# Optimization experiments

Measured on AMD Instinct MI355X. Metric: run time of the kernel, lower is better.

## Reference

```python
import jax, jax.numpy as jnp
import numpy as np

N_NODES = 100000
N_EDGES = 1600000
D_IN = 128
D_HID = 128


def setup_inputs() -> dict:
    key = jax.random.key(0)
    ks = jax.random.split(key, 8)
    x = jax.random.normal(ks[0], (N_NODES, D_IN), dtype=jnp.float32)
    edge_index = jax.random.randint(ks[1], (2, N_EDGES), 0, N_NODES, dtype=jnp.int64)
    def glorot(k, fan_in, fan_out):
        s = jnp.sqrt(6.0 / (fan_in + fan_out))
        return jax.random.uniform(k, (fan_in, fan_out), jnp.float32, -s, s)
    return {
        "x": x,
        "edge_index": edge_index,
        "W1": glorot(ks[2], D_IN, D_HID), "b1": jnp.zeros((D_HID,), jnp.float32),
        "W2": glorot(ks[3], D_HID, D_HID), "b2": jnp.zeros((D_HID,), jnp.float32),
        "W3": glorot(ks[4], D_HID, D_HID), "b3": jnp.zeros((D_HID,), jnp.float32),
    }


def _gcn_conv(x, src, dst, norm, W, b, n_nodes):
    # x: [N, d_in] -> [N, d_out]; PyG GCNConv: scatter(norm * (xW)[src] -> dst) + b
    h = x @ W                                    # [N, d_out]
    msg = h[src] * norm[:, None]                 # [E+N, d_out] gathered messages
    out = jax.ops.segment_sum(msg, dst, num_segments=n_nodes)
    return out + b


def _norm_and_loops(edge_index, n_nodes):
    # add self-loops, compute symmetric normalization deg^-1/2[src]*deg^-1/2[dst]
    loop = jnp.arange(n_nodes, dtype=edge_index.dtype)
    src = jnp.concatenate([edge_index[0], loop])
    dst = jnp.concatenate([edge_index[1], loop])
    deg = jax.ops.segment_sum(jnp.ones_like(dst, dtype=jnp.float32), dst,
                              num_segments=n_nodes)
    dinv = jnp.where(deg > 0, jax.lax.rsqrt(deg), 0.0)
    norm = dinv[src] * dinv[dst]                 # [E+N]
    return src, dst, norm


def reference(x, edge_index, W1, b1, W2, b2, W3, b3):
    n = x.shape[0]
    src, dst, norm = _norm_and_loops(edge_index, n)
    h = jax.nn.relu(_gcn_conv(x, src, dst, norm, W1, b1, n))
    h = jax.nn.relu(_gcn_conv(h, src, dst, norm, W2, b2, n))
    return _gcn_conv(h, src, dst, norm, W3, b3, n)
```

## Files before the change

### kernel.cpp

```cpp
#include <hip/hip_runtime.h>

#define D 128

typedef __attribute__((ext_vector_type(8))) short bf16x8;
typedef __attribute__((ext_vector_type(4))) float f32x4;

union Frag {
    unsigned short s[8];
    uint4 u;
    bf16x8 v;
};

__device__ inline unsigned short bf16_rne(float x) {
    unsigned u = __float_as_uint(x);
    return (unsigned short)((u + 0x7fffu + ((u >> 16) & 1)) >> 16);
}

__global__ void detect64_k(const int* __restrict__ raw, int* __restrict__ flag) {
    __shared__ int bad;
    if (threadIdx.x == 0) bad = 0;
    __syncthreads();
    for (int i = threadIdx.x; i < 4096; i += 256)
        if (raw[2 * i + 1] != 0) bad = 1;
    __syncthreads();
    if (threadIdx.x == 0) *flag = bad ? 0 : 1;
}

__global__ void hist_k(const int* __restrict__ raw, const int* __restrict__ flag,
                       int* __restrict__ cnt, int E) {
    bool is64 = (*flag != 0);
    int S = gridDim.x * blockDim.x;
    int i = blockIdx.x * blockDim.x + threadIdx.x;
    for (; i + 3 * S < E; i += 4 * S) {
        int d0 = is64 ? raw[2 * (E + i)]         : raw[E + i];
        int d1 = is64 ? raw[2 * (E + i + S)]     : raw[E + i + S];
        int d2 = is64 ? raw[2 * (E + i + 2 * S)] : raw[E + i + 2 * S];
        int d3 = is64 ? raw[2 * (E + i + 3 * S)] : raw[E + i + 3 * S];
        atomicAdd(&cnt[d0], 1);
        atomicAdd(&cnt[d1], 1);
        atomicAdd(&cnt[d2], 1);
        atomicAdd(&cnt[d3], 1);
    }
    for (; i < E; i += S) {
        int d = is64 ? raw[2 * (E + i)] : raw[E + i];
        atomicAdd(&cnt[d], 1);
    }
}

__global__ void dinv_k(const int* __restrict__ cnt, float* __restrict__ dinv, int n) {
    int i = blockIdx.x * blockDim.x + threadIdx.x;
    if (i < n) dinv[i] = rsqrtf((float)cnt[i] + 1.0f);
}

__global__ void scan1_k(const int* __restrict__ cnt, int* __restrict__ rp,
                        int* __restrict__ part, int n) {
    __shared__ int s[256];
    int t = threadIdx.x;
    int base = blockIdx.x * 1024 + t * 4;
    int v0 = 0, v1 = 0, v2 = 0, v3 = 0;
    if (base + 0 < n) v0 = cnt[base + 0];
    if (base + 1 < n) v1 = cnt[base + 1];
    if (base + 2 < n) v2 = cnt[base + 2];
    if (base + 3 < n) v3 = cnt[base + 3];
    int sum = v0 + v1 + v2 + v3;
    s[t] = sum;
    __syncthreads();
    for (int off = 1; off < 256; off <<= 1) {
        int xv = 0;
        if (t >= off) xv = s[t - off];
        __syncthreads();
        s[t] += xv;
        __syncthreads();
    }
    int run = s[t] - sum;
    if (base + 0 < n) rp[base + 0] = run; run += v0;
    if (base + 1 < n) rp[base + 1] = run; run += v1;
    if (base + 2 < n) rp[base + 2] = run; run += v2;
    if (base + 3 < n) rp[base + 3] = run;
    if (t == 255) part[blockIdx.x] = s[255];
}

__global__ void scan2_k(int* __restrict__ part, int nb) {
    if (nb <= 256) {
        __shared__ int s[256];
        int t = threadIdx.x;
        int v = (t < nb) ? part[t] : 0;
        s[t] = v;
        __syncthreads();
        for (int off = 1; off < 256; off <<= 1) {
            int xv = 0;
            if (t >= off) xv = s[t - off];
            __syncthreads();
            s[t] += xv;
            __syncthreads();
        }
        if (t < nb) part[t] = s[t] - v;
    } else if (threadIdx.x == 0) {
        int run = 0;
        for (int i = 0; i < nb; i++) { int v = part[i]; part[i] = run; run += v; }
    }
}

__global__ void scan3_k(int* __restrict__ rp, int* __restrict__ cursor,
                        const int* __restrict__ part, int n, int E) {
    int i = blockIdx.x * blockDim.x + threadIdx.x;
    if (i < n) {
        int v = rp[i] + part[i >> 10];
        rp[i] = v;
        cursor[i] = v;
    }
    if (i == 0) rp[n] = E;
}

__global__ void build_k(const int* __restrict__ raw, const int* __restrict__ flag,
                        const float* __restrict__ dinv,
                        int* __restrict__ cursor, int2* __restrict__ csr, int E) {
    bool is64 = (*flag != 0);
    int S = gridDim.x * blockDim.x;
    int i = blockIdx.x * blockDim.x + threadIdx.x;
    for (; i + 3 * S < E; i += 4 * S) {
        int i0 = i, i1 = i + S, i2 = i + 2 * S, i3 = i + 3 * S;
        int s0 = is64 ? raw[2 * i0] : raw[i0];
        int s1 = is64 ? raw[2 * i1] : raw[i1];
        int s2 = is64 ? raw[2 * i2] : raw[i2];
        int s3 = is64 ? raw[2 * i3] : raw[i3];
        int d0 = is64 ? raw[2 * (E + i0)] : raw[E + i0];
        int d1 = is64 ? raw[2 * (E + i1)] : raw[E + i1];
        int d2 = is64 ? raw[2 * (E + i2)] : raw[E + i2];
        int d3 = is64 ? raw[2 * (E + i3)] : raw[E + i3];
        int p0 = atomicAdd(&cursor[d0], 1);
        int p1 = atomicAdd(&cursor[d1], 1);
        int p2 = atomicAdd(&cursor[d2], 1);
        int p3 = atomicAdd(&cursor[d3], 1);
        float w0 = dinv[s0] * dinv[d0];
        float w1 = dinv[s1] * dinv[d1];
        float w2 = dinv[s2] * dinv[d2];
        float w3 = dinv[s3] * dinv[d3];
        csr[p0] = make_int2(s0, __float_as_int(w0));
        csr[p1] = make_int2(s1, __float_as_int(w1));
        csr[p2] = make_int2(s2, __float_as_int(w2));
        csr[p3] = make_int2(s3, __float_as_int(w3));
    }
    for (; i < E; i += S) {
        int s = is64 ? raw[2 * i] : raw[i];
        int d = is64 ? raw[2 * (E + i)] : raw[E + i];
        int pos = atomicAdd(&cursor[d], 1);
        float w = dinv[s] * dinv[d];
        csr[pos] = make_int2(s, __float_as_int(w));
    }
}

__global__ void pack_k(const float* __restrict__ W, uint4* __restrict__ whi,
                       uint4* __restrict__ wlo) {
    int id = blockIdx.x * 256 + threadIdx.x;
    if (id >= 2048) return;
    int lane = id & 63, st = id >> 6;
    int s = st >> 3, t = st & 7;
    int col = t * 16 + (lane & 15);
    int kb = s * 32 + ((lane >> 4) & 3) * 8;
    Frag H, L;
#pragma unroll
    for (int j = 0; j < 8; ++j) {
        float x = W[(size_t)(kb + j) * D + col];
        unsigned u = __float_as_uint(x);
        unsigned r = (u + 0x7fffu + ((u >> 16) & 1)) & 0xffff0000u;
        H.s[j] = (unsigned short)(r >> 16);
        L.s[j] = bf16_rne(x - __uint_as_float(r));
    }
    whi[st * 64 + lane] = H.u;
    wlo[st * 64 + lane] = L.u;
}

template <int PRE>
__global__ __launch_bounds__(256) void gemm_mfma_k(const float* __restrict__ A,
        const uint4* __restrict__ whi, const uint4* __restrict__ wlo,
        float* __restrict__ H, int M) {
    int wv = threadIdx.x >> 6, lane = threadIdx.x & 63;
    int row0 = blockIdx.x * 64 + wv * 16;
    int arow = row0 + (lane & 15);
    if (arow >= M) arow = M - 1;
    const float* ap = A + (size_t)arow * D + ((lane >> 4) & 3) * 8;
    f32x4 acc[8];
#pragma unroll
    for (int t = 0; t < 8; ++t) acc[t] = (f32x4){0.f, 0.f, 0.f, 0.f};
#pragma unroll
    for (int s = 0; s < 4; ++s) {
        float4 a0 = *(const float4*)(ap + s * 32);
        float4 a1 = *(const float4*)(ap + s * 32 + 4);
        float av[8] = {a0.x, a0.y, a0.z, a0.w, a1.x, a1.y, a1.z, a1.w};
        Frag Ah, Al;
#pragma unroll
        for (int j = 0; j < 8; ++j) {
            float x = av[j];
            if (PRE) x = fmaxf(x, 0.f);
            unsigned u = __float_as_uint(x);
            unsigned r = (u + 0x7fffu + ((u >> 16) & 1)) & 0xffff0000u;
            Ah.s[j] = (unsigned short)(r >> 16);
            Al.s[j] = bf16_rne(x - __uint_as_float(r));
        }
        const uint4* wh = whi + (size_t)s * 8 * 64 + lane;
        const uint4* wl = wlo + (size_t)s * 8 * 64 + lane;
#pragma unroll
        for (int t = 0; t < 8; ++t) {
            Frag Bh, Bl;
            Bh.u = wh[t * 64];
            Bl.u = wl[t * 64];
            acc[t] = __builtin_amdgcn_mfma_f32_16x16x32_bf16(Ah.v, Bh.v, acc[t], 0, 0, 0);
            acc[t] = __builtin_amdgcn_mfma_f32_16x16x32_bf16(Al.v, Bh.v, acc[t], 0, 0, 0);
            acc[t] = __builtin_amdgcn_mfma_f32_16x16x32_bf16(Ah.v, Bl.v, acc[t], 0, 0, 0);
        }
    }
    int g = (lane >> 4) & 3, c = lane & 15;
#pragma unroll
    for (int r = 0; r < 4; ++r) {
        int row = row0 + g * 4 + r;
        if (row < M) {
#pragma unroll
            for (int t = 0; t < 8; ++t)
                H[(size_t)row * D + t * 16 + c] = acc[t][r];
        }
    }
}

__global__ __launch_bounds__(256) void agg_k(const float* __restrict__ h,
                                             const float* __restrict__ dinv,
                                             const int* __restrict__ rp,
                                             const int2* __restrict__ csr,
                                             const float* __restrict__ bias,
                                             float* __restrict__ out, int n) {
    int node = (blockIdx.x << 2) + (threadIdx.x >> 6);
    int lane = threadIdx.x & 63;
    if (node >= n) return;
    const float2* h2 = (const float2*)h;
    float2 b2 = ((const float2*)bias)[lane];
    float dn = dinv[node];
    float2 hv = h2[(size_t)node * 64 + lane];
    float sl = dn * dn;
    float accx = b2.x + sl * hv.x;
    float accy = b2.y + sl * hv.y;
    int e = rp[node], e1 = rp[node + 1];
    for (; e + 8 <= e1; e += 8) {
        int2 p0 = csr[e + 0], p1 = csr[e + 1], p2 = csr[e + 2], p3 = csr[e + 3];
        int2 p4 = csr[e + 4], p5 = csr[e + 5], p6 = csr[e + 6], p7 = csr[e + 7];
        float2 v0 = h2[(size_t)p0.x * 64 + lane];
        float2 v1 = h2[(size_t)p1.x * 64 + lane];
        float2 v2 = h2[(size_t)p2.x * 64 + lane];
        float2 v3 = h2[(size_t)p3.x * 64 + lane];
        float2 v4 = h2[(size_t)p4.x * 64 + lane];
        float2 v5 = h2[(size_t)p5.x * 64 + lane];
        float2 v6 = h2[(size_t)p6.x * 64 + lane];
        float2 v7 = h2[(size_t)p7.x * 64 + lane];
        float w0 = __int_as_float(p0.y), w1 = __int_as_float(p1.y);
        float w2 = __int_as_float(p2.y), w3 = __int_as_float(p3.y);
        float w4 = __int_as_float(p4.y), w5 = __int_as_float(p5.y);
        float w6 = __int_as_float(p6.y), w7 = __int_as_float(p7.y);
        accx += w0 * v0.x + w1 * v1.x + w2 * v2.x + w3 * v3.x
              + w4 * v4.x + w5 * v5.x + w6 * v6.x + w7 * v7.x;
        accy += w0 * v0.y + w1 * v1.y + w2 * v2.y + w3 * v3.y
              + w4 * v4.y + w5 * v5.y + w6 * v6.y + w7 * v7.y;
    }
    for (; e + 4 <= e1; e += 4) {
        int2 p0 = csr[e + 0], p1 = csr[e + 1], p2 = csr[e + 2], p3 = csr[e + 3];
        float2 v0 = h2[(size_t)p0.x * 64 + lane];
        float2 v1 = h2[(size_t)p1.x * 64 + lane];
        float2 v2 = h2[(size_t)p2.x * 64 + lane];
        float2 v3 = h2[(size_t)p3.x * 64 + lane];
        float w0 = __int_as_float(p0.y), w1 = __int_as_float(p1.y);
        float w2 = __int_as_float(p2.y), w3 = __int_as_float(p3.y);
        accx += w0 * v0.x + w1 * v1.x + w2 * v2.x + w3 * v3.x;
        accy += w0 * v0.y + w1 * v1.y + w2 * v2.y + w3 * v3.y;
    }
    for (; e < e1; ++e) {
        int2 p0 = csr[e];
        float w0 = __int_as_float(p0.y);
        float2 v0 = h2[(size_t)p0.x * 64 + lane];
        accx += w0 * v0.x;
        accy += w0 * v0.y;
    }
    float2 o; o.x = accx; o.y = accy;
    ((float2*)out)[(size_t)node * 64 + lane] = o;
}

extern "C" void kernel_launch(void* const* d_in, const int* in_sizes, int n_in,
                              void* d_out, int out_size, void* d_ws, size_t ws_size,
                              hipStream_t stream) {
    const float* x  = (const float*)d_in[0];
    const int* eraw = (const int*)d_in[1];
    const float* W1 = (const float*)d_in[2];
    const float* b1 = (const float*)d_in[3];
    const float* W2 = (const float*)d_in[4];
    const float* b2 = (const float*)d_in[5];
    const float* W3 = (const float*)d_in[6];
    const float* b3 = (const float*)d_in[7];
    int N = in_sizes[0] / D;
    int E = in_sizes[1] / 2;
    float* out = (float*)d_out;

    char* w = (char*)d_ws;
    float* h    = (float*)w; w += (size_t)N * D * 4;
    int2* csr   = (int2*)w;  w += (size_t)E * 8;
    int* cnt    = (int*)w;   w += (size_t)N * 4;
    float* dinv = (float*)w; w += (size_t)N * 4;
    int* rp     = (int*)w;   w += (size_t)(N + 1) * 4;
    int* cursor = (int*)w;   w += (size_t)N * 4;
    int* part   = (int*)w;   w += 1024 * 4;
    int* flag   = (int*)w;   w += 16;
    uint4* whi[3]; uint4* wlo[3];
    for (int l = 0; l < 3; ++l) {
        whi[l] = (uint4*)w; w += 2048 * 16;
        wlo[l] = (uint4*)w; w += 2048 * 16;
    }

    detect64_k<<<1, 256, 0, stream>>>(eraw, flag);
    hipMemsetAsync(cnt, 0, (size_t)N * 4, stream);
    hist_k<<<512, 256, 0, stream>>>(eraw, flag, cnt, E);
    dinv_k<<<(N + 255) / 256, 256, 0, stream>>>(cnt, dinv, N);
    int nb = (N + 1023) / 1024;
    scan1_k<<<nb, 256, 0, stream>>>(cnt, rp, part, N);
    scan2_k<<<1, 256, 0, stream>>>(part, nb);
    scan3_k<<<(N + 255) / 256, 256, 0, stream>>>(rp, cursor, part, N, E);
    build_k<<<512, 256, 0, stream>>>(eraw, flag, dinv, cursor, csr, E);

    pack_k<<<8, 256, 0, stream>>>(W1, whi[0], wlo[0]);
    pack_k<<<8, 256, 0, stream>>>(W2, whi[1], wlo[1]);
    pack_k<<<8, 256, 0, stream>>>(W3, whi[2], wlo[2]);

    int gb = (N + 63) / 64;
    int ab = (N + 3) / 4;
    gemm_mfma_k<0><<<gb, 256, 0, stream>>>(x, whi[0], wlo[0], h, N);
    agg_k<<<ab, 256, 0, stream>>>(h, dinv, rp, csr, b1, out, N);
    gemm_mfma_k<1><<<gb, 256, 0, stream>>>(out, whi[1], wlo[1], h, N);
    agg_k<<<ab, 256, 0, stream>>>(h, dinv, rp, csr, b2, out, N);
    gemm_mfma_k<1><<<gb, 256, 0, stream>>>(out, whi[2], wlo[2], h, N);
    agg_k<<<ab, 256, 0, stream>>>(h, dinv, rp, csr, b3, out, N);
}
```

Measured before the change: 739.5 us.

## Store intermediate features in bf16 and shrink CSR to source-only indices

The GEMM output h is now written as bf16, which halves the bytes the gather-heavy aggregation reads per neighbor. The CSR drops the precomputed edge weight and stores only the source index; aggregation recomputes the weight as dinv[src]*dinv[node], trading an extra small gather for less CSR traffic. The three weight-packing launches are merged into one, and the 4-edge unrolled tail loop is removed. Rounding h to bf16 loses precision and could push results close to the tolerance.

```diff
diff --git a/kernel.cpp b/kernel.cpp
--- a/kernel.cpp
+++ b/kernel.cpp
@@ -113,8 +113,7 @@
 }
 
 __global__ void build_k(const int* __restrict__ raw, const int* __restrict__ flag,
-                        const float* __restrict__ dinv,
-                        int* __restrict__ cursor, int2* __restrict__ csr, int E) {
+                        int* __restrict__ cursor, int* __restrict__ csr, int E) {
     bool is64 = (*flag != 0);
     int S = gridDim.x * blockDim.x;
     int i = blockIdx.x * blockDim.x + threadIdx.x;
@@ -132,28 +131,27 @@
         int p1 = atomicAdd(&cursor[d1], 1);
         int p2 = atomicAdd(&cursor[d2], 1);
         int p3 = atomicAdd(&cursor[d3], 1);
-        float w0 = dinv[s0] * dinv[d0];
-        float w1 = dinv[s1] * dinv[d1];
-        float w2 = dinv[s2] * dinv[d2];
-        float w3 = dinv[s3] * dinv[d3];
-        csr[p0] = make_int2(s0, __float_as_int(w0));
-        csr[p1] = make_int2(s1, __float_as_int(w1));
-        csr[p2] = make_int2(s2, __float_as_int(w2));
-        csr[p3] = make_int2(s3, __float_as_int(w3));
+        csr[p0] = s0;
+        csr[p1] = s1;
+        csr[p2] = s2;
+        csr[p3] = s3;
     }
     for (; i < E; i += S) {
         int s = is64 ? raw[2 * i] : raw[i];
         int d = is64 ? raw[2 * (E + i)] : raw[E + i];
         int pos = atomicAdd(&cursor[d], 1);
-        float w = dinv[s] * dinv[d];
-        csr[pos] = make_int2(s, __float_as_int(w));
-    }
-}
-
-__global__ void pack_k(const float* __restrict__ W, uint4* __restrict__ whi,
-                       uint4* __restrict__ wlo) {
-    int id = blockIdx.x * 256 + threadIdx.x;
-    if (id >= 2048) return;
+        csr[pos] = s;
+    }
+}
+
+__global__ void pack_k(const float* __restrict__ W1f, const float* __restrict__ W2f,
+                       const float* __restrict__ W3f, uint4* __restrict__ wbuf) {
+    int gid = blockIdx.x * 256 + threadIdx.x;
+    int layer = gid >> 11;
+    int id = gid & 2047;
+    const float* W = layer == 0 ? W1f : (layer == 1 ? W2f : W3f);
+    uint4* whi = wbuf + (size_t)layer * 4096;
+    uint4* wlo = whi + 2048;
     int lane = id & 63, st = id >> 6;
     int s = st >> 3, t = st & 7;
     int col = t * 16 + (lane & 15);
@@ -174,7 +172,7 @@
 template <int PRE>
 __global__ __launch_bounds__(256) void gemm_mfma_k(const float* __restrict__ A,
         const uint4* __restrict__ whi, const uint4* __restrict__ wlo,
-        float* __restrict__ H, int M) {
+        unsigned short* __restrict__ H, int M) {
     int wv = threadIdx.x >> 6, lane = threadIdx.x & 63;
     int row0 = blockIdx.x * 64 + wv * 16;
     int arow = row0 + (lane & 15);
@@ -217,65 +215,57 @@
         if (row < M) {
 #pragma unroll
             for (int t = 0; t < 8; ++t)
-                H[(size_t)row * D + t * 16 + c] = acc[t][r];
+                H[(size_t)row * D + t * 16 + c] = bf16_rne(acc[t][r]);
         }
     }
 }
 
-__global__ __launch_bounds__(256) void agg_k(const float* __restrict__ h,
+__global__ __launch_bounds__(256) void agg_k(const unsigned int* __restrict__ hu,
                                              const float* __restrict__ dinv,
                                              const int* __restrict__ rp,
-                                             const int2* __restrict__ csr,
+                                             const int* __restrict__ csr,
                                              const float* __restrict__ bias,
                                              float* __restrict__ out, int n) {
     int node = (blockIdx.x << 2) + (threadIdx.x >> 6);
     int lane = threadIdx.x & 63;
     if (node >= n) return;
-    const float2* h2 = (const float2*)h;
     float2 b2 = ((const float2*)bias)[lane];
     float dn = dinv[node];
-    float2 hv = h2[(size_t)node * 64 + lane];
+    unsigned hv = hu[(size_t)node * 64 + lane];
     float sl = dn * dn;
-    float accx = b2.x + sl * hv.x;
-    float accy = b2.y + sl * hv.y;
+    float accx = b2.x + sl * __uint_as_float(hv << 16);
+    float accy = b2.y + sl * __uint_as_float(hv & 0xffff0000u);
     int e = rp[node], e1 = rp[node + 1];
     for (; e + 8 <= e1; e += 8) {
-        int2 p0 = csr[e + 0], p1 = csr[e + 1], p2 = csr[e + 2], p3 = csr[e + 3];
-        int2 p4 = csr[e + 4], p5 = csr[e + 5], p6 = csr[e + 6], p7 = csr[e + 7];
-        float2 v0 = h2[(size_t)p0.x * 64 + lane];
-        float2 v1 = h2[(size_t)p1.x * 64 + lane];
-        float2 v2 = h2[(size_t)p2.x * 64 + lane];
-        float2 v3 = h2[(size_t)p3.x * 64 + lane];
-        float2 v4 = h2[(size_t)p4.x * 64 + lane];
-        float2 v5 = h2[(size_t)p5.x * 64 + lane];
-        float2 v6 = h2[(size_t)p6.x * 64 + lane];
-        float2 v7 = h2[(size_t)p7.x * 64 + lane];
-        float w0 = __int_as_float(p0.y), w1 = __int_as_float(p1.y);
-        float w2 = __int_as_float(p2.y), w3 = __int_as_float(p3.y);
-        float w4 = __int_as_float(p4.y), w5 = __int_as_float(p5.y);
-        float w6 = __int_as_float(p6.y), w7 = __int_as_float(p7.y);
-        accx += w0 * v0.x + w1 * v1.x + w2 * v2.x + w3 * v3.x
-              + w4 * v4.x + w5 * v5.x + w6 * v6.x + w7 * v7.x;
-        accy += w0 * v0.y + w1 * v1.y + w2 * v2.y + w3 * v3.y
-              + w4 * v4.y + w5 * v5.y + w6 * v6.y + w7 * v7.y;
-    }
-    for (; e + 4 <= e1; e += 4) {
-        int2 p0 = csr[e + 0], p1 = csr[e + 1], p2 = csr[e + 2], p3 = csr[e + 3];
-        float2 v0 = h2[(size_t)p0.x * 64 + lane];
-        float2 v1 = h2[(size_t)p1.x * 64 + lane];
-        float2 v2 = h2[(size_t)p2.x * 64 + lane];
-        float2 v3 = h2[(size_t)p3.x * 64 + lane];
-        float w0 = __int_as_float(p0.y), w1 = __int_as_float(p1.y);
-        float w2 = __int_as_float(p2.y), w3 = __int_as_float(p3.y);
-        accx += w0 * v0.x + w1 * v1.x + w2 * v2.x + w3 * v3.x;
-        accy += w0 * v0.y + w1 * v1.y + w2 * v2.y + w3 * v3.y;
+        int s0 = csr[e + 0], s1 = csr[e + 1], s2 = csr[e + 2], s3 = csr[e + 3];
+        int s4 = csr[e + 4], s5 = csr[e + 5], s6 = csr[e + 6], s7 = csr[e + 7];
+        unsigned u0 = hu[(size_t)s0 * 64 + lane];
+        unsigned u1 = hu[(size_t)s1 * 64 + lane];
+        unsigned u2 = hu[(size_t)s2 * 64 + lane];
+        unsigned u3 = hu[(size_t)s3 * 64 + lane];
+        unsigned u4 = hu[(size_t)s4 * 64 + lane];
+        unsigned u5 = hu[(size_t)s5 * 64 + lane];
+        unsigned u6 = hu[(size_t)s6 * 64 + lane];
+        unsigned u7 = hu[(size_t)s7 * 64 + lane];
+        float w0 = dinv[s0] * dn, w1 = dinv[s1] * dn;
+        float w2 = dinv[s2] * dn, w3 = dinv[s3] * dn;
+        float w4 = dinv[s4] * dn, w5 = dinv[s5] * dn;
+        float w6 = dinv[s6] * dn, w7 = dinv[s7] * dn;
+        accx += w0 * __uint_as_float(u0 << 16) + w1 * __uint_as_float(u1 << 16)
+              + w2 * __uint_as_float(u2 << 16) + w3 * __uint_as_float(u3 << 16)
+              + w4 * __uint_as_float(u4 << 16) + w5 * __uint_as_float(u5 << 16)
+              + w6 * __uint_as_float(u6 << 16) + w7 * __uint_as_float(u7 << 16);
+        accy += w0 * __uint_as_float(u0 & 0xffff0000u) + w1 * __uint_as_float(u1 & 0xffff0000u)
+              + w2 * __uint_as_float(u2 & 0xffff0000u) + w3 * __uint_as_float(u3 & 0xffff0000u)
+              + w4 * __uint_as_float(u4 & 0xffff0000u) + w5 * __uint_as_float(u5 & 0xffff0000u)
+              + w6 * __uint_as_float(u6 & 0xffff0000u) + w7 * __uint_as_float(u7 & 0xffff0000u);
     }
     for (; e < e1; ++e) {
-        int2 p0 = csr[e];
-        float w0 = __int_as_float(p0.y);
-        float2 v0 = h2[(size_t)p0.x * 64 + lane];
-        accx += w0 * v0.x;
-        accy += w0 * v0.y;
+        int s0 = csr[e];
+        float w0 = dinv[s0] * dn;
+        unsigned u0 = hu[(size_t)s0 * 64 + lane];
+        accx += w0 * __uint_as_float(u0 << 16);
+        accy += w0 * __uint_as_float(u0 & 0xffff0000u);
     }
     float2 o; o.x = accx; o.y = accy;
     ((float2*)out)[(size_t)node * 64 + lane] = o;
@@ -297,19 +287,15 @@
     float* out = (float*)d_out;
 
     char* w = (char*)d_ws;
-    float* h    = (float*)w; w += (size_t)N * D * 4;
-    int2* csr   = (int2*)w;  w += (size_t)E * 8;
+    unsigned int* h = (unsigned int*)w; w += (size_t)N * D * 2;
+    int* csr    = (int*)w;   w += (size_t)E * 4;
     int* cnt    = (int*)w;   w += (size_t)N * 4;
     float* dinv = (float*)w; w += (size_t)N * 4;
     int* rp     = (int*)w;   w += (size_t)(N + 1) * 4;
     int* cursor = (int*)w;   w += (size_t)N * 4;
     int* part   = (int*)w;   w += 1024 * 4;
     int* flag   = (int*)w;   w += 16;
-    uint4* whi[3]; uint4* wlo[3];
-    for (int l = 0; l < 3; ++l) {
-        whi[l] = (uint4*)w; w += 2048 * 16;
-        wlo[l] = (uint4*)w; w += 2048 * 16;
-    }
+    uint4* wbuf = (uint4*)w; w += 3 * 4096 * 16;
 
     detect64_k<<<1, 256, 0, stream>>>(eraw, flag);
     hipMemsetAsync(cnt, 0, (size_t)N * 4, stream);
@@ -319,18 +305,19 @@
     scan1_k<<<nb, 256, 0, stream>>>(cnt, rp, part, N);
     scan2_k<<<1, 256, 0, stream>>>(part, nb);
     scan3_k<<<(N + 255) / 256, 256, 0, stream>>>(rp, cursor, part, N, E);
-    build_k<<<512, 256, 0, stream>>>(eraw, flag, dinv, cursor, csr, E);
-
-    pack_k<<<8, 256, 0, stream>>>(W1, whi[0], wlo[0]);
-    pack_k<<<8, 256, 0, stream>>>(W2, whi[1], wlo[1]);
-    pack_k<<<8, 256, 0, stream>>>(W3, whi[2], wlo[2]);
+    build_k<<<512, 256, 0, stream>>>(eraw, flag, cursor, csr, E);
+
+    pack_k<<<24, 256, 0, stream>>>(W1, W2, W3, wbuf);
 
     int gb = (N + 63) / 64;
     int ab = (N + 3) / 4;
-    gemm_mfma_k<0><<<gb, 256, 0, stream>>>(x, whi[0], wlo[0], h, N);
+    uint4* whi1 = wbuf, *wlo1 = wbuf + 2048;
+    uint4* whi2 = wbuf + 4096, *wlo2 = wbuf + 6144;
+    uint4* whi3 = wbuf + 8192, *wlo3 = wbuf + 10240;
+    gemm_mfma_k<0><<<gb, 256, 0, stream>>>(x, whi1, wlo1, (unsigned short*)h, N);
     agg_k<<<ab, 256, 0, stream>>>(h, dinv, rp, csr, b1, out, N);
-    gemm_mfma_k<1><<<gb, 256, 0, stream>>>(out, whi[1], wlo[1], h, N);
+    gemm_mfma_k<1><<<gb, 256, 0, stream>>>(out, whi2, wlo2, (unsigned short*)h, N);
     agg_k<<<ab, 256, 0, stream>>>(h, dinv, rp, csr, b2, out, N);
-    gemm_mfma_k<1><<<gb, 256, 0, stream>>>(out, whi[2], wlo[2], h, N);
+    gemm_mfma_k<1><<<gb, 256, 0, stream>>>(out, whi3, wlo3, (unsigned short*)h, N);
     agg_k<<<ab, 256, 0, stream>>>(h, dinv, rp, csr, b3, out, N);
 }
```

Measured after the change: 603.9 us. 18.3% less time.
